# Kernel optimization log

Hardware: AMD Instinct MI355X
Metric: run time of the kernel (lower is better)

Reference implementation:

```python
import jax, jax.numpy as jnp
import numpy as np

B, T, DIM, MDIM, HID = 16, 2048, 1024, 128, 512
WIN = 16
HALF = WIN // 2              # 8 even / 8 odd tokens per window
MAXP = int(0.8 * HALF)       # candidate_ratio * min(nA, nB) = 6 pairs per window
SIM_THRESH = -10.0           # permissive: never masks a cosine similarity
KEEP_RATIO = 0.7
SIM_W, IMP_W, ALPHA_SCALE = 1.0, 0.5, 5.0
LN_EPS = 1e-5


def _ln(x, g, b):
    mu = jnp.mean(x, -1, keepdims=True)
    var = jnp.mean((x - mu) ** 2, -1, keepdims=True)
    return (x - mu) / jnp.sqrt(var + LN_EPS) * g + b


def _greedy(s):
    # s: [HALF, HALF] bipartite sims. Greedy conflict-free matching by descending
    # similarity; since min(nA,nB)=8 >= MAXP=6 it always yields exactly MAXP pairs.
    order = jnp.argsort(-s.reshape(-1))

    def body(k, st):
        usedA, usedB, pa, pb, cnt = st
        idx = order[k]
        iA = (idx // HALF).astype(jnp.int32)
        iB = (idx % HALF).astype(jnp.int32)
        ok = (cnt < MAXP) & (~usedA[iA]) & (~usedB[iB])
        usedA = usedA.at[iA].set(usedA[iA] | ok)
        usedB = usedB.at[iB].set(usedB[iB] | ok)
        w = jnp.where(ok, cnt, MAXP)  # slot MAXP is a scratch slot
        pa = pa.at[w].set(jnp.where(ok, iA, pa[w]))
        pb = pb.at[w].set(jnp.where(ok, iB, pb[w]))
        return (usedA, usedB, pa, pb, cnt + ok.astype(jnp.int32))

    st0 = (jnp.zeros(HALF, bool), jnp.zeros(HALF, bool),
           jnp.zeros(MAXP + 1, jnp.int32), jnp.zeros(MAXP + 1, jnp.int32),
           jnp.int32(0))
    _, _, pa, pb, _ = jax.lax.fori_loop(0, HALF * HALF, body, st0)
    pa, pb = pa[:MAXP], pb[:MAXP]
    return pa, pb, s[pa, pb]


def _forward(x, ln_m_g, ln_m_b, w_match, ln_i_g, ln_i_b, w_imp1, b_imp1, w_imp2, b_imp2):
    Bc, Tc, C = x.shape
    nW = Tc // WIN
    P = nW * MAXP
    K = int((1.0 - KEEP_RATIO) * Tc)  # fixed merge budget (top-K)

    # matching space (L2-normalized) and per-token importance
    m = _ln(x, ln_m_g, ln_m_b) @ w_match                      # [B,T,MDIM]
    m = m / jnp.linalg.norm(m, axis=-1, keepdims=True)
    h = jax.nn.relu(_ln(x, ln_i_g, ln_i_b) @ w_imp1 + b_imp1)
    imp = jax.nn.sigmoid((h @ w_imp2 + b_imp2)[..., 0])       # [B,T]

    # windowed even/odd bipartite similarity
    mw = m.reshape(Bc, nW, WIN, MDIM)
    sim = jnp.einsum('bwad,bwcd->bwac', mw[:, :, 0::2], mw[:, :, 1::2])  # [B,nW,8,8]
    sim = jnp.where(sim < SIM_THRESH, -jnp.inf, sim)

    pa, pb, sv = jax.vmap(jax.vmap(_greedy))(sim)             # [B,nW,MAXP]
    wstart = (jnp.arange(nW, dtype=jnp.int32) * WIN)[None, :, None]
    i_idx = (wstart + 2 * pa).reshape(Bc, P)                  # keep token (even)
    j_idx = (wstart + 2 * pb + 1).reshape(Bc, P)              # drop token (odd)
    sim_c = sv.reshape(Bc, P)
    imp_i = jnp.take_along_axis(imp, i_idx, axis=1)
    imp_j = jnp.take_along_axis(imp, j_idx, axis=1)

    # fixed budget: exactly top-K merges by score (high sim, low importance)
    scores = SIM_W * sim_c - IMP_W * 0.5 * (imp_i + imp_j)
    _, top = jax.lax.top_k(scores, K)
    z = jnp.zeros((Bc, P), x.dtype).at[jnp.arange(Bc)[:, None], top].set(1.0)

    # merge keeps i, drops j; alpha from relative importance
    alpha = jax.nn.sigmoid(ALPHA_SCALE * (imp_i - imp_j))[..., None]
    xi = jnp.take_along_axis(x, i_idx[..., None], axis=1)
    xj = jnp.take_along_axis(x, j_idx[..., None], axis=1)
    merged = alpha * xi + (1.0 - alpha) * xj                  # [B,P,C]

    def pack_one(xb, ib, jb, mb, zb):
        # i indices are globally unique -> scatter merged content where z==1
        x_new = xb.at[ib].add(zb[:, None] * (mb - xb[ib]))
        drop = (jnp.zeros(Tc, xb.dtype).at[jb].add(zb)) > 0.5
        # stable argsort keeps surviving tokens in time order; take first T-K
        order = jnp.argsort(drop.astype(jnp.int32))[:Tc - K]
        return x_new[order]

    return jax.vmap(pack_one)(x, i_idx, j_idx, merged, z)     # [B, T-K, C]


def setup_inputs() -> dict:
    key = jax.random.key(0)
    ks = jax.random.split(key, 4)
    s = 0.02
    return {
        'x': jax.random.normal(ks[0], (B, T, DIM), jnp.float32),
        'ln_m_g': jnp.ones((DIM,), jnp.float32),
        'ln_m_b': jnp.zeros((DIM,), jnp.float32),
        'w_match': jax.random.normal(ks[1], (DIM, MDIM), jnp.float32) * s,
        'ln_i_g': jnp.ones((DIM,), jnp.float32),
        'ln_i_b': jnp.zeros((DIM,), jnp.float32),
        'w_imp1': jax.random.normal(ks[2], (DIM, HID), jnp.float32) * s,
        'b_imp1': jnp.zeros((HID,), jnp.float32),
        'w_imp2': jax.random.normal(ks[3], (HID, 1), jnp.float32) * s,
        'b_imp2': jnp.zeros((1,), jnp.float32),
    }


def reference(x, ln_m_g, ln_m_b, w_match, ln_i_g, ln_i_b, w_imp1, b_imp1, w_imp2, b_imp2):
    return _forward(x, ln_m_g, ln_m_b, w_match, ln_i_g, ln_i_b, w_imp1, b_imp1, w_imp2, b_imp2)
```

## Files before the change

### kernel.cpp

```cpp
#include <hip/hip_runtime.h>
#include <math.h>

#define B_ 16
#define T_ 2048
#define DIM_ 1024
#define MDIM_ 128
#define HID_ 512
#define NCAT 640
#define NW_ 128
#define WINSZ 16
#define MAXP_ 6
#define P_ 768
#define KDROP 614
#define TKEEP 1434
#define NTOK (B_*T_)

typedef unsigned short u16;
typedef __bf16 bf16x8 __attribute__((ext_vector_type(8)));
typedef float f32x4 __attribute__((ext_vector_type(4)));
typedef unsigned short us4 __attribute__((ext_vector_type(4)));

#define OFF_WCAT   0
#define OFF_BIAS   (OFF_WCAT + DIM_*NCAT)
#define OFF_MU     (OFF_BIAS + NCAT)
#define OFF_RS     (OFF_MU + NTOK)
#define OFF_MBUF   (OFF_RS + NTOK)
#define OFF_LOGIT  (OFF_MBUF + NTOK*MDIM_)
#define OFF_IMP    (OFF_LOGIT + NTOK)
#define OFF_IIDX   (OFF_IMP + NTOK)
#define OFF_JIDX   (OFF_IIDX + B_*P_)
#define OFF_SV     (OFF_JIDX + B_*P_)
#define OFF_ALPHA  (OFF_SV + B_*P_)
#define OFF_REP    (OFF_ALPHA + B_*P_)
#define OFF_DROP   (OFF_REP + NTOK)
#define OFF_POS    (OFF_DROP + NTOK)

static constexpr size_t F_AH    = 0;
static constexpr size_t F_AL    = F_AH + (size_t)NTOK*DIM_/2;
static constexpr size_t F_BH    = F_AL + (size_t)NTOK*DIM_/2;
static constexpr size_t F_BL    = F_BH + (size_t)NCAT*DIM_/2;
static constexpr size_t F_BIAS  = F_BL + (size_t)NCAT*DIM_/2;
static constexpr size_t F_MBUF  = F_BIAS + NCAT;
static constexpr size_t F_LOGIT = F_MBUF + (size_t)NTOK*MDIM_;
static constexpr size_t F_IMP   = F_LOGIT + NTOK;
static constexpr size_t F_IIDX  = F_IMP + NTOK;
static constexpr size_t F_JIDX  = F_IIDX + (size_t)B_*P_;
static constexpr size_t F_SV    = F_JIDX + (size_t)B_*P_;
static constexpr size_t F_ALPHA = F_SV + (size_t)B_*P_;
static constexpr size_t F_REP   = F_ALPHA + (size_t)B_*P_;
static constexpr size_t F_DROP  = F_REP + NTOK;
static constexpr size_t F_POS   = F_DROP + NTOK;
static constexpr size_t F_TOTAL = F_POS + NTOK;

__device__ __forceinline__ u16 f2bf(float f) {
  unsigned u = __builtin_bit_cast(unsigned, f);
  unsigned r = u + 0x7FFFu + ((u >> 16) & 1u);
  return (u16)(r >> 16);
}
__device__ __forceinline__ float bf2f(u16 h) {
  unsigned u = ((unsigned)h) << 16;
  return __builtin_bit_cast(float, u);
}
__device__ __forceinline__ void gll16(const void* g, void* l) {
  __builtin_amdgcn_global_load_lds((const __attribute__((address_space(1))) void*)g,
                                   (__attribute__((address_space(3))) void*)l, 16, 0, 0);
}


__global__ __launch_bounds__(256) void prep_a(const float* __restrict__ x,
    u16* __restrict__ Ah, u16* __restrict__ Al) {
  int token = blockIdx.x * 4 + (threadIdx.x >> 6);
  int lane = threadIdx.x & 63;
  const float4* xr = (const float4*)(x + (size_t)token * DIM_);
  float4 v[4];
  float sum = 0.f;
#pragma unroll
  for (int it = 0; it < 4; ++it) {
    v[it] = xr[lane + it * 64];
    sum += v[it].x + v[it].y + v[it].z + v[it].w;
  }
  for (int o = 32; o > 0; o >>= 1) sum += __shfl_xor(sum, o);
  float m = sum * (1.f / 1024.f);
  float ss = 0.f;
#pragma unroll
  for (int it = 0; it < 4; ++it) {
    float a = v[it].x - m, b = v[it].y - m, c = v[it].z - m, d = v[it].w - m;
    ss += a * a + b * b + c * c + d * d;
  }
  for (int o = 32; o > 0; o >>= 1) ss += __shfl_xor(ss, o);
  float rsv = 1.0f / sqrtf(ss * (1.f / 1024.f) + 1e-5f);
#pragma unroll
  for (int it = 0; it < 4; ++it) {
    float e[4] = {(v[it].x - m) * rsv, (v[it].y - m) * rsv,
                  (v[it].z - m) * rsv, (v[it].w - m) * rsv};
    us4 hv, lv;
#pragma unroll
    for (int j = 0; j < 4; ++j) {
      u16 h = f2bf(e[j]);
      hv[j] = h;
      lv[j] = f2bf(e[j] - bf2f(h));
    }
    size_t off = (size_t)token * DIM_ + (size_t)(lane + it * 64) * 4;
    *(us4*)&Ah[off] = hv;
    *(us4*)&Al[off] = lv;
  }
}

__global__ __launch_bounds__(256) void prep_b(const float* __restrict__ wm,
    const float* __restrict__ wi, const float* __restrict__ gm,
    const float* __restrict__ gi, u16* __restrict__ Bh, u16* __restrict__ Bl) {
  int e = blockIdx.x * 256 + threadIdx.x;
  if (e >= NCAT * DIM_) return;
  int n = e >> 10, k = e & 1023;
  float wv = (n < MDIM_) ? gm[k] * wm[k * MDIM_ + n]
                         : gi[k] * wi[k * HID_ + (n - MDIM_)];
  u16 h = f2bf(wv);
  Bh[e] = h;
  Bl[e] = f2bf(wv - bf2f(h));
}

__global__ __launch_bounds__(256, 2) void gemm_mfma(
    const u16* __restrict__ Ah, const u16* __restrict__ Al,
    const u16* __restrict__ Bh, const u16* __restrict__ Bl,
    const float* __restrict__ biascat, const float* __restrict__ w2,
    float* __restrict__ mbuf, float* __restrict__ logit) {
  __shared__ __align__(16) u16 sAH[8 * 512];
  __shared__ __align__(16) u16 sAL[8 * 512];
  __shared__ __align__(16) u16 sBH[8 * 512];
  __shared__ __align__(16) u16 sBL[8 * 512];
  const int tid = threadIdx.x;
  const int w = tid >> 6, lane = tid & 63;
  int bid = blockIdx.x;
  int q = bid / 40, rem = bid % 40;
  int ct = rem >> 3, x8 = rem & 7;
  int stripe = x8 + 8 * q;
  const int row0 = stripe * 128, col0 = ct * 128;
  const int wy = w >> 1, wx = w & 1;
  const int m16 = lane & 15, quad = lane >> 4;

  const u16* gA = (w == 0) ? Ah : (w == 1) ? Al : (w == 2) ? Bh : Bl;
  u16* lds0 = ((w == 0) ? sAH : (w == 1) ? sAL : (w == 2) ? sBH : sBL) + lane * 8;
  const int rbase = (w < 2) ? row0 : col0;
  const u16* gsrc0 = gA + (size_t)(rbase + m16) * DIM_ + quad * 8;

  f32x4 acc[4][4] = {};
  for (int k0 = 0; k0 < DIM_; k0 += 32) {
    __syncthreads();
#pragma unroll
    for (int t = 0; t < 8; ++t)
      gll16(gsrc0 + (size_t)t * 16 * DIM_ + k0, lds0 + t * 512);
    __syncthreads();
    bf16x8 ah[4], al[4], bh[4], bl[4];
#pragma unroll
    for (int i = 0; i < 4; ++i) {
      ah[i] = *(const bf16x8*)&sAH[(wy * 4 + i) * 512 + lane * 8];
      al[i] = *(const bf16x8*)&sAL[(wy * 4 + i) * 512 + lane * 8];
      bh[i] = *(const bf16x8*)&sBH[(wx * 4 + i) * 512 + lane * 8];
      bl[i] = *(const bf16x8*)&sBL[(wx * 4 + i) * 512 + lane * 8];
    }
#pragma unroll
    for (int i = 0; i < 4; ++i)
#pragma unroll
      for (int j = 0; j < 4; ++j) {
        acc[i][j] = __builtin_amdgcn_mfma_f32_16x16x32_bf16(ah[i], bh[j], acc[i][j], 0, 0, 0);
        acc[i][j] = __builtin_amdgcn_mfma_f32_16x16x32_bf16(ah[i], bl[j], acc[i][j], 0, 0, 0);
        acc[i][j] = __builtin_amdgcn_mfma_f32_16x16x32_bf16(al[i], bh[j], acc[i][j], 0, 0, 0);
      }
  }
  if (ct == 0) {
#pragma unroll
    for (int i = 0; i < 4; ++i)
#pragma unroll
      for (int j = 0; j < 4; ++j) {
        int col = wx * 64 + j * 16 + m16;
        float bs = biascat[col];
#pragma unroll
        for (int r = 0; r < 4; ++r) {
          int row = row0 + wy * 64 + i * 16 + quad * 4 + r;
          mbuf[(size_t)row * MDIM_ + col] = acc[i][j][r] + bs;
        }
      }
  } else {
#pragma unroll
    for (int i = 0; i < 4; ++i) {
      float part[4] = {0.f, 0.f, 0.f, 0.f};
#pragma unroll
      for (int j = 0; j < 4; ++j) {
        int col = col0 + wx * 64 + j * 16 + m16;
        float bs = biascat[col];
        float wv = w2[col - MDIM_];
#pragma unroll
        for (int r = 0; r < 4; ++r) {
          float v = acc[i][j][r] + bs;
          v = v > 0.f ? v : 0.f;
          part[r] += v * wv;
        }
      }
#pragma unroll
      for (int r = 0; r < 4; ++r) {
        part[r] += __shfl_xor(part[r], 1);
        part[r] += __shfl_xor(part[r], 2);
        part[r] += __shfl_xor(part[r], 4);
        part[r] += __shfl_xor(part[r], 8);
      }
      if (m16 == 0)
#pragma unroll
        for (int r = 0; r < 4; ++r)
          atomicAdd(&logit[row0 + wy * 64 + i * 16 + quad * 4 + r], part[r]);
    }
  }
}


__global__ __launch_bounds__(256) void build_bias(const float* __restrict__ wm,
    const float* __restrict__ wi, const float* __restrict__ bm,
    const float* __restrict__ bi, const float* __restrict__ b1,
    float* __restrict__ biascat) {
  int c = blockIdx.x;
  float s = 0.f;
  for (int k = threadIdx.x; k < DIM_; k += 256)
    s += (c < MDIM_) ? bm[k] * wm[k * MDIM_ + c]
                     : bi[k] * wi[k * HID_ + (c - MDIM_)];
  __shared__ float red[256];
  red[threadIdx.x] = s; __syncthreads();
  for (int o = 128; o > 0; o >>= 1) {
    if (threadIdx.x < o) red[threadIdx.x] += red[threadIdx.x + o];
    __syncthreads();
  }
  if (threadIdx.x == 0)
    biascat[c] = red[0] + ((c >= MDIM_) ? b1[c - MDIM_] : 0.f);
}

__global__ void zero_logit(float* __restrict__ logit) {
  int i = blockIdx.x * 256 + threadIdx.x;
  if (i < NTOK) logit[i] = 0.f;
}

__global__ __launch_bounds__(256) void norm_m(float* __restrict__ mbuf) {
  int token = blockIdx.x * 4 + (threadIdx.x >> 6);
  int lane = threadIdx.x & 63;
  float2* mr = (float2*)(mbuf + (size_t)token * MDIM_);
  float2 v = mr[lane];
  float ss = v.x * v.x + v.y * v.y;
  for (int o = 32; o > 0; o >>= 1) ss += __shfl_xor(ss, o);
  float inv = 1.0f / sqrtf(ss);
  v.x *= inv; v.y *= inv;
  mr[lane] = v;
}

__global__ void imp_kernel(const float* __restrict__ logit,
    const float* __restrict__ b2, float* __restrict__ imp) {
  int i = blockIdx.x * 256 + threadIdx.x;
  if (i < NTOK) {
    float z = logit[i] + b2[0];
    imp[i] = 1.f / (1.f + expf(-z));
  }
}

__global__ __launch_bounds__(256) void simgreedy(const float* __restrict__ mbuf,
    int* __restrict__ ii, int* __restrict__ jj, float* __restrict__ sv) {
  __shared__ __align__(16) float sm[4][16][132];
  int wv = threadIdx.x >> 6, lane = threadIdx.x & 63;
  int win = blockIdx.x * 4 + wv;
  int b = win >> 7, w = win & 127;
  size_t base = ((size_t)b * T_ + w * WINSZ) * MDIM_;
#pragma unroll
  for (int it = 0; it < 8; ++it) {
    int e4 = it * 64 + lane;
    int row = e4 >> 5, c4 = e4 & 31;
    float4 v = *(const float4*)(mbuf + base + (size_t)row * MDIM_ + c4 * 4);
    *(float4*)&sm[wv][row][c4 * 4] = v;
  }
  __syncthreads();
  int a = lane >> 3, c = lane & 7;
  const float* ev = sm[wv][2 * a];
  const float* od = sm[wv][2 * c + 1];
  float s = 0.f;
#pragma unroll
  for (int k = 0; k < MDIM_; ++k) s += ev[k] * od[k];
  if (s < -10.0f) s = -__builtin_inff();
  float v = s;
  bool alive = true;
  int outb = (b * NW_ + w) * MAXP_;
  for (int p = 0; p < MAXP_; ++p) {
    float bv = alive ? v : -__builtin_inff();
    int bi = lane;
    for (int o = 32; o > 0; o >>= 1) {
      float ov = __shfl_xor(bv, o);
      int oi = __shfl_xor(bi, o);
      if (ov > bv || (ov == bv && oi < bi)) { bv = ov; bi = oi; }
    }
    int wa = bi >> 3, wc = bi & 7;
    if (lane == 0) {
      ii[outb + p] = w * WINSZ + 2 * wa;
      jj[outb + p] = w * WINSZ + 2 * wc + 1;
      sv[outb + p] = bv;
    }
    if (a == wa || c == wc) alive = false;
  }
}

__global__ __launch_bounds__(256) void select_kernel(const float* __restrict__ sv,
    const int* __restrict__ ii, const int* __restrict__ jj,
    const float* __restrict__ imp, float* __restrict__ alpha,
    int* __restrict__ rep, int* __restrict__ drop) {
  int b = blockIdx.x, tid = threadIdx.x;
  __shared__ float sc[P_];
  for (int t = tid; t < T_; t += 256) {
    rep[b * T_ + t] = -1;
    drop[b * T_ + t] = 0;
  }
  for (int p = tid; p < P_; p += 256) {
    int i = ii[b * P_ + p], j = jj[b * P_ + p];
    float fi = imp[b * T_ + i], fj = imp[b * T_ + j];
    sc[p] = sv[b * P_ + p] - 0.25f * (fi + fj);
    alpha[b * P_ + p] = 1.f / (1.f + expf(-5.f * (fi - fj)));
  }
  __syncthreads();
  for (int p = tid; p < P_; p += 256) {
    float s = sc[p];
    int cnt = 0;
    for (int q = 0; q < P_; ++q) {
      float t = sc[q];
      cnt += (t > s) || (t == s && q < p);
    }
    if (cnt < KDROP) {
      rep[b * T_ + ii[b * P_ + p]] = p;
      drop[b * T_ + jj[b * P_ + p]] = 1;
    }
  }
}

__global__ __launch_bounds__(64) void prefix_kernel(const int* __restrict__ drop,
    int* __restrict__ pos) {
  int b = blockIdx.x, lane = threadIdx.x;
  const int* dr = drop + b * T_;
  int t0 = lane * 32;
  int s = 0;
  for (int k = 0; k < 32; ++k) s += (dr[t0 + k] ? 0 : 1);
  int incl = s;
  for (int o = 1; o < 64; o <<= 1) {
    int n = __shfl_up(incl, o);
    if (lane >= o) incl += n;
  }
  int run = incl - s;
  int* ps = pos + b * T_;
  for (int k = 0; k < 32; ++k) {
    ps[t0 + k] = run;
    run += (dr[t0 + k] ? 0 : 1);
  }
}

__global__ __launch_bounds__(256) void pack_kernel(const float* __restrict__ x,
    const int* __restrict__ drop, const int* __restrict__ pos,
    const int* __restrict__ rep, const float* __restrict__ alpha,
    const int* __restrict__ jj, float* __restrict__ out) {
  int t = blockIdx.x, b = blockIdx.y;
  if (drop[b * T_ + t]) return;
  int tid = threadIdx.x;
  const float4* xi = (const float4*)(x + ((size_t)b * T_ + t) * DIM_);
  float4 v = xi[tid];
  int p = rep[b * T_ + t];
  if (p >= 0) {
    float a = alpha[b * P_ + p];
    int j = jj[b * P_ + p];
    const float4* xj = (const float4*)(x + ((size_t)b * T_ + j) * DIM_);
    float4 vj = xj[tid];
    v.x = a * v.x + (1.f - a) * vj.x;
    v.y = a * v.y + (1.f - a) * vj.y;
    v.z = a * v.z + (1.f - a) * vj.z;
    v.w = a * v.w + (1.f - a) * vj.w;
  }
  int np = pos[b * T_ + t];
  ((float4*)(out + ((size_t)b * TKEEP + np) * DIM_))[tid] = v;
}


__global__ __launch_bounds__(256) void build_wcat(const float* __restrict__ wm,
    const float* __restrict__ wi, const float* __restrict__ gm,
    const float* __restrict__ gi, float* __restrict__ Wcat) {
  int e = blockIdx.x * 256 + threadIdx.x;
  if (e >= DIM_ * NCAT) return;
  int k = e / NCAT, c = e - k * NCAT;
  float v = (c < MDIM_) ? gm[k] * wm[k * MDIM_ + c]
                        : gi[k] * wi[k * HID_ + (c - MDIM_)];
  Wcat[e] = v;
}

__global__ __launch_bounds__(256) void ln_stats(const float* __restrict__ x,
    float* __restrict__ mu, float* __restrict__ rs) {
  int token = blockIdx.x * 4 + (threadIdx.x >> 6);
  int lane = threadIdx.x & 63;
  const float4* xr = (const float4*)(x + (size_t)token * DIM_);
  float4 v[4];
  float sum = 0.f;
#pragma unroll
  for (int it = 0; it < 4; ++it) {
    v[it] = xr[lane + it * 64];
    sum += v[it].x + v[it].y + v[it].z + v[it].w;
  }
  for (int o = 32; o > 0; o >>= 1) sum += __shfl_xor(sum, o);
  float m = sum * (1.f / 1024.f);
  float ss = 0.f;
#pragma unroll
  for (int it = 0; it < 4; ++it) {
    float a = v[it].x - m, b = v[it].y - m, c = v[it].z - m, d = v[it].w - m;
    ss += a * a + b * b + c * c + d * d;
  }
  for (int o = 32; o > 0; o >>= 1) ss += __shfl_xor(ss, o);
  if (lane == 0) {
    mu[token] = m;
    rs[token] = 1.0f / sqrtf(ss * (1.f / 1024.f) + 1e-5f);
  }
}

__global__ __launch_bounds__(256) void gemm640(const float* __restrict__ x,
    const float* __restrict__ mu, const float* __restrict__ rs,
    const float* __restrict__ Wcat, const float* __restrict__ biascat,
    const float* __restrict__ w2, float* __restrict__ mbuf,
    float* __restrict__ logit) {
  __shared__ __align__(16) float As[16][68];
  __shared__ __align__(16) float Bs[16][68];
  const int tid = threadIdx.x;
  const int row0 = blockIdx.x * 64, col0 = blockIdx.y * 64;
  const int tx = tid & 15, ty = tid >> 4;
  const int arow = tid >> 2, akk = (tid & 3) << 2;
  const int brow = tid >> 4, bnn = (tid & 15) << 2;
  const int t_g = row0 + arow;
  const float tmu = mu[t_g], trs = rs[t_g];
  const float* xrow = x + (size_t)t_g * DIM_ + akk;
  const float* wptr = Wcat + (size_t)brow * NCAT + col0 + bnn;
  float acc[4][4] = {};
  for (int k0 = 0; k0 < DIM_; k0 += 16) {
    float4 av = *(const float4*)(xrow + k0);
    float4 bv = *(const float4*)(wptr + (size_t)k0 * NCAT);
    As[akk + 0][arow] = (av.x - tmu) * trs;
    As[akk + 1][arow] = (av.y - tmu) * trs;
    As[akk + 2][arow] = (av.z - tmu) * trs;
    As[akk + 3][arow] = (av.w - tmu) * trs;
    *(float4*)&Bs[brow][bnn] = bv;
    __syncthreads();
#pragma unroll
    for (int k = 0; k < 16; ++k) {
      float4 a = *(const float4*)&As[k][ty << 2];
      float4 b = *(const float4*)&Bs[k][tx << 2];
      acc[0][0] += a.x * b.x; acc[0][1] += a.x * b.y; acc[0][2] += a.x * b.z; acc[0][3] += a.x * b.w;
      acc[1][0] += a.y * b.x; acc[1][1] += a.y * b.y; acc[1][2] += a.y * b.z; acc[1][3] += a.y * b.w;
      acc[2][0] += a.z * b.x; acc[2][1] += a.z * b.y; acc[2][2] += a.z * b.z; acc[2][3] += a.z * b.w;
      acc[3][0] += a.w * b.x; acc[3][1] += a.w * b.y; acc[3][2] += a.w * b.z; acc[3][3] += a.w * b.w;
    }
    __syncthreads();
  }
  float bias[4];
#pragma unroll
  for (int j = 0; j < 4; ++j) bias[j] = biascat[col0 + (tx << 2) + j];
  if (col0 < MDIM_) {
#pragma unroll
    for (int i = 0; i < 4; ++i) {
      int t = row0 + (ty << 2) + i;
      float4 o;
      o.x = acc[i][0] + bias[0]; o.y = acc[i][1] + bias[1];
      o.z = acc[i][2] + bias[2]; o.w = acc[i][3] + bias[3];
      *(float4*)(mbuf + (size_t)t * MDIM_ + col0 + (tx << 2)) = o;
    }
  } else {
    float w2v[4];
#pragma unroll
    for (int j = 0; j < 4; ++j) w2v[j] = w2[col0 - MDIM_ + (tx << 2) + j];
#pragma unroll
    for (int i = 0; i < 4; ++i) {
      float p = 0.f;
#pragma unroll
      for (int j = 0; j < 4; ++j) {
        float v = acc[i][j] + bias[j];
        v = v > 0.f ? v : 0.f;
        p += v * w2v[j];
      }
      p += __shfl_xor(p, 1); p += __shfl_xor(p, 2);
      p += __shfl_xor(p, 4); p += __shfl_xor(p, 8);
      if (tx == 0) atomicAdd(&logit[row0 + (ty << 2) + i], p);
    }
  }
}

extern "C" void kernel_launch(void* const* d_in, const int* in_sizes, int n_in,
                              void* d_out, int out_size, void* d_ws, size_t ws_size,
                              hipStream_t stream) {
  const float* x    = (const float*)d_in[0];
  const float* gm   = (const float*)d_in[1];
  const float* bm   = (const float*)d_in[2];
  const float* wm   = (const float*)d_in[3];
  const float* gi   = (const float*)d_in[4];
  const float* bi   = (const float*)d_in[5];
  const float* wi   = (const float*)d_in[6];
  const float* b1   = (const float*)d_in[7];
  const float* w2   = (const float*)d_in[8];
  const float* b2   = (const float*)d_in[9];
  float* ws = (float*)d_ws;
  float* out = (float*)d_out;

  if (ws_size >= F_TOTAL * sizeof(float)) {
    u16* Ah = (u16*)(ws + F_AH);
    u16* Al = (u16*)(ws + F_AL);
    u16* Bh = (u16*)(ws + F_BH);
    u16* Bl = (u16*)(ws + F_BL);
    float* bias  = ws + F_BIAS;
    float* mbuf  = ws + F_MBUF;
    float* logit = ws + F_LOGIT;
    float* imp   = ws + F_IMP;
    int* iidx    = (int*)(ws + F_IIDX);
    int* jidx    = (int*)(ws + F_JIDX);
    float* sv    = ws + F_SV;
    float* alpha = ws + F_ALPHA;
    int* rep     = (int*)(ws + F_REP);
    int* drop    = (int*)(ws + F_DROP);
    int* pos     = (int*)(ws + F_POS);

    prep_b<<<(NCAT * DIM_ + 255) / 256, 256, 0, stream>>>(wm, wi, gm, gi, Bh, Bl);
    build_bias<<<NCAT, 256, 0, stream>>>(wm, wi, bm, bi, b1, bias);
    zero_logit<<<NTOK / 256, 256, 0, stream>>>(logit);
    prep_a<<<NTOK / 4, 256, 0, stream>>>(x, Ah, Al);
    gemm_mfma<<<(NTOK / 128) * (NCAT / 128), 256, 0, stream>>>(Ah, Al, Bh, Bl, bias, w2, mbuf, logit);
    norm_m<<<NTOK / 4, 256, 0, stream>>>(mbuf);
    imp_kernel<<<NTOK / 256, 256, 0, stream>>>(logit, b2, imp);
    simgreedy<<<(B_ * NW_) / 4, 256, 0, stream>>>(mbuf, iidx, jidx, sv);
    select_kernel<<<B_, 256, 0, stream>>>(sv, iidx, jidx, imp, alpha, rep, drop);
    prefix_kernel<<<B_, 64, 0, stream>>>(drop, pos);
    dim3 pgrid(T_, B_);
    pack_kernel<<<pgrid, 256, 0, stream>>>(x, drop, pos, rep, alpha, jidx, out);
  } else {
    float* Wcat = ws + OFF_WCAT;
    float* bias = ws + OFF_BIAS;
    float* mu   = ws + OFF_MU;
    float* rs   = ws + OFF_RS;
    float* mbuf = ws + OFF_MBUF;
    float* logit = ws + OFF_LOGIT;
    float* imp  = ws + OFF_IMP;
    int* iidx   = (int*)(ws + OFF_IIDX);
    int* jidx   = (int*)(ws + OFF_JIDX);
    float* sv   = ws + OFF_SV;
    float* alpha = ws + OFF_ALPHA;
    int* rep    = (int*)(ws + OFF_REP);
    int* drop   = (int*)(ws + OFF_DROP);
    int* pos    = (int*)(ws + OFF_POS);

    build_wcat<<<(DIM_ * NCAT + 255) / 256, 256, 0, stream>>>(wm, wi, gm, gi, Wcat);
    build_bias<<<NCAT, 256, 0, stream>>>(wm, wi, bm, bi, b1, bias);
    zero_logit<<<NTOK / 256, 256, 0, stream>>>(logit);
    ln_stats<<<NTOK / 4, 256, 0, stream>>>(x, mu, rs);
    dim3 ggrid(NTOK / 64, NCAT / 64);
    gemm640<<<ggrid, 256, 0, stream>>>(x, mu, rs, Wcat, bias, w2, mbuf, logit);
    norm_m<<<NTOK / 4, 256, 0, stream>>>(mbuf);
    imp_kernel<<<NTOK / 256, 256, 0, stream>>>(logit, b2, imp);
    simgreedy<<<(B_ * NW_) / 4, 256, 0, stream>>>(mbuf, iidx, jidx, sv);
    select_kernel<<<B_, 256, 0, stream>>>(sv, iidx, jidx, imp, alpha, rep, drop);
    prefix_kernel<<<B_, 64, 0, stream>>>(drop, pos);
    dim3 pgrid(T_, B_);
    pack_kernel<<<pgrid, 256, 0, stream>>>(x, drop, pos, rep, alpha, jidx, out);
  }
}
```

Measured before the change: 573.5 us.

## Double-buffer GEMM LDS tiles and fuse small kernels into neighbors

The MFMA GEMM gets double-buffered LDS tiles, so the global-to-LDS load for the next K slice is issued before the current slice's math and one barrier per iteration goes away. Several small kernels are folded into neighbours: weight prep and bias build share one launch, and L2 normalisation moves into simgreedy's shared-memory stage. The sigmoid importance and the prefix scan move into the selection kernel, and zeroing uses hipMemsetAsync. This cuts launch count and global round-trips, at the cost of doubled LDS per GEMM block, which may lower occupancy.

```diff
diff --git a/kernel.cpp b/kernel.cpp
--- a/kernel.cpp
+++ b/kernel.cpp
@@ -26,8 +26,7 @@
 #define OFF_RS     (OFF_MU + NTOK)
 #define OFF_MBUF   (OFF_RS + NTOK)
 #define OFF_LOGIT  (OFF_MBUF + NTOK*MDIM_)
-#define OFF_IMP    (OFF_LOGIT + NTOK)
-#define OFF_IIDX   (OFF_IMP + NTOK)
+#define OFF_IIDX   (OFF_LOGIT + NTOK)
 #define OFF_JIDX   (OFF_IIDX + B_*P_)
 #define OFF_SV     (OFF_JIDX + B_*P_)
 #define OFF_ALPHA  (OFF_SV + B_*P_)
@@ -42,8 +41,7 @@
 static constexpr size_t F_BIAS  = F_BL + (size_t)NCAT*DIM_/2;
 static constexpr size_t F_MBUF  = F_BIAS + NCAT;
 static constexpr size_t F_LOGIT = F_MBUF + (size_t)NTOK*MDIM_;
-static constexpr size_t F_IMP   = F_LOGIT + NTOK;
-static constexpr size_t F_IIDX  = F_IMP + NTOK;
+static constexpr size_t F_IIDX  = F_LOGIT + NTOK;
 static constexpr size_t F_JIDX  = F_IIDX + (size_t)B_*P_;
 static constexpr size_t F_SV    = F_JIDX + (size_t)B_*P_;
 static constexpr size_t F_ALPHA = F_SV + (size_t)B_*P_;
@@ -106,17 +104,36 @@
   }
 }
 
-__global__ __launch_bounds__(256) void prep_b(const float* __restrict__ wm,
+__global__ __launch_bounds__(256) void prep_w(const float* __restrict__ wm,
     const float* __restrict__ wi, const float* __restrict__ gm,
-    const float* __restrict__ gi, u16* __restrict__ Bh, u16* __restrict__ Bl) {
-  int e = blockIdx.x * 256 + threadIdx.x;
-  if (e >= NCAT * DIM_) return;
-  int n = e >> 10, k = e & 1023;
-  float wv = (n < MDIM_) ? gm[k] * wm[k * MDIM_ + n]
-                         : gi[k] * wi[k * HID_ + (n - MDIM_)];
-  u16 h = f2bf(wv);
-  Bh[e] = h;
-  Bl[e] = f2bf(wv - bf2f(h));
+    const float* __restrict__ gi, const float* __restrict__ bm,
+    const float* __restrict__ bi, const float* __restrict__ b1,
+    u16* __restrict__ Bh, u16* __restrict__ Bl, float* __restrict__ biascat) {
+  int bid = blockIdx.x;
+  const int NBLK_B = (NCAT * DIM_) / 256;
+  if (bid < NBLK_B) {
+    int e = bid * 256 + threadIdx.x;
+    int n = e >> 10, k = e & 1023;
+    float wv = (n < MDIM_) ? gm[k] * wm[k * MDIM_ + n]
+                           : gi[k] * wi[k * HID_ + (n - MDIM_)];
+    u16 h = f2bf(wv);
+    Bh[e] = h;
+    Bl[e] = f2bf(wv - bf2f(h));
+  } else {
+    int c = bid - NBLK_B;
+    float s = 0.f;
+    for (int k = threadIdx.x; k < DIM_; k += 256)
+      s += (c < MDIM_) ? bm[k] * wm[k * MDIM_ + c]
+                       : bi[k] * wi[k * HID_ + (c - MDIM_)];
+    __shared__ float red[256];
+    red[threadIdx.x] = s; __syncthreads();
+    for (int o = 128; o > 0; o >>= 1) {
+      if (threadIdx.x < o) red[threadIdx.x] += red[threadIdx.x + o];
+      __syncthreads();
+    }
+    if (threadIdx.x == 0)
+      biascat[c] = red[0] + ((c >= MDIM_) ? b1[c - MDIM_] : 0.f);
+  }
 }
 
 __global__ __launch_bounds__(256, 2) void gemm_mfma(
@@ -124,10 +141,10 @@
     const u16* __restrict__ Bh, const u16* __restrict__ Bl,
     const float* __restrict__ biascat, const float* __restrict__ w2,
     float* __restrict__ mbuf, float* __restrict__ logit) {
-  __shared__ __align__(16) u16 sAH[8 * 512];
-  __shared__ __align__(16) u16 sAL[8 * 512];
-  __shared__ __align__(16) u16 sBH[8 * 512];
-  __shared__ __align__(16) u16 sBL[8 * 512];
+  __shared__ __align__(16) u16 sAH[2][8 * 512];
+  __shared__ __align__(16) u16 sAL[2][8 * 512];
+  __shared__ __align__(16) u16 sBH[2][8 * 512];
+  __shared__ __align__(16) u16 sBL[2][8 * 512];
   const int tid = threadIdx.x;
   const int w = tid >> 6, lane = tid & 63;
   int bid = blockIdx.x;
@@ -139,24 +156,32 @@
   const int m16 = lane & 15, quad = lane >> 4;
 
   const u16* gA = (w == 0) ? Ah : (w == 1) ? Al : (w == 2) ? Bh : Bl;
-  u16* lds0 = ((w == 0) ? sAH : (w == 1) ? sAL : (w == 2) ? sBH : sBL) + lane * 8;
+  u16* lds0 = ((w == 0) ? sAH[0] : (w == 1) ? sAL[0] : (w == 2) ? sBH[0] : sBL[0]) + lane * 8;
+  u16* lds1 = ((w == 0) ? sAH[1] : (w == 1) ? sAL[1] : (w == 2) ? sBH[1] : sBL[1]) + lane * 8;
   const int rbase = (w < 2) ? row0 : col0;
   const u16* gsrc0 = gA + (size_t)(rbase + m16) * DIM_ + quad * 8;
 
+#pragma unroll
+  for (int t = 0; t < 8; ++t)
+    gll16(gsrc0 + (size_t)t * 16 * DIM_, lds0 + t * 512);
+
   f32x4 acc[4][4] = {};
-  for (int k0 = 0; k0 < DIM_; k0 += 32) {
+  for (int k0 = 0; k0 < 32; ++k0) {
     __syncthreads();
-#pragma unroll
-    for (int t = 0; t < 8; ++t)
-      gll16(gsrc0 + (size_t)t * 16 * DIM_ + k0, lds0 + t * 512);
-    __syncthreads();
+    if (k0 + 1 < 32) {
+      u16* nb = (k0 & 1) ? lds0 : lds1;
+#pragma unroll
+      for (int t = 0; t < 8; ++t)
+        gll16(gsrc0 + (size_t)t * 16 * DIM_ + (k0 + 1) * 32, nb + t * 512);
+    }
+    const int cb = k0 & 1;
     bf16x8 ah[4], al[4], bh[4], bl[4];
 #pragma unroll
     for (int i = 0; i < 4; ++i) {
-      ah[i] = *(const bf16x8*)&sAH[(wy * 4 + i) * 512 + lane * 8];
-      al[i] = *(const bf16x8*)&sAL[(wy * 4 + i) * 512 + lane * 8];
-      bh[i] = *(const bf16x8*)&sBH[(wx * 4 + i) * 512 + lane * 8];
-      bl[i] = *(const bf16x8*)&sBL[(wx * 4 + i) * 512 + lane * 8];
+      ah[i] = *(const bf16x8*)&sAH[cb][(wy * 4 + i) * 512 + lane * 8];
+      al[i] = *(const bf16x8*)&sAL[cb][(wy * 4 + i) * 512 + lane * 8];
+      bh[i] = *(const bf16x8*)&sBH[cb][(wx * 4 + i) * 512 + lane * 8];
+      bl[i] = *(const bf16x8*)&sBL[cb][(wx * 4 + i) * 512 + lane * 8];
     }
 #pragma unroll
     for (int i = 0; i < 4; ++i)
@@ -212,51 +237,6 @@
 }
 
 
-__global__ __launch_bounds__(256) void build_bias(const float* __restrict__ wm,
-    const float* __restrict__ wi, const float* __restrict__ bm,
-    const float* __restrict__ bi, const float* __restrict__ b1,
-    float* __restrict__ biascat) {
-  int c = blockIdx.x;
-  float s = 0.f;
-  for (int k = threadIdx.x; k < DIM_; k += 256)
-    s += (c < MDIM_) ? bm[k] * wm[k * MDIM_ + c]
-                     : bi[k] * wi[k * HID_ + (c - MDIM_)];
-  __shared__ float red[256];
-  red[threadIdx.x] = s; __syncthreads();
-  for (int o = 128; o > 0; o >>= 1) {
-    if (threadIdx.x < o) red[threadIdx.x] += red[threadIdx.x + o];
-    __syncthreads();
-  }
-  if (threadIdx.x == 0)
-    biascat[c] = red[0] + ((c >= MDIM_) ? b1[c - MDIM_] : 0.f);
-}
-
-__global__ void zero_logit(float* __restrict__ logit) {
-  int i = blockIdx.x * 256 + threadIdx.x;
-  if (i < NTOK) logit[i] = 0.f;
-}
-
-__global__ __launch_bounds__(256) void norm_m(float* __restrict__ mbuf) {
-  int token = blockIdx.x * 4 + (threadIdx.x >> 6);
-  int lane = threadIdx.x & 63;
-  float2* mr = (float2*)(mbuf + (size_t)token * MDIM_);
-  float2 v = mr[lane];
-  float ss = v.x * v.x + v.y * v.y;
-  for (int o = 32; o > 0; o >>= 1) ss += __shfl_xor(ss, o);
-  float inv = 1.0f / sqrtf(ss);
-  v.x *= inv; v.y *= inv;
-  mr[lane] = v;
-}
-
-__global__ void imp_kernel(const float* __restrict__ logit,
-    const float* __restrict__ b2, float* __restrict__ imp) {
-  int i = blockIdx.x * 256 + threadIdx.x;
-  if (i < NTOK) {
-    float z = logit[i] + b2[0];
-    imp[i] = 1.f / (1.f + expf(-z));
-  }
-}
-
 __global__ __launch_bounds__(256) void simgreedy(const float* __restrict__ mbuf,
     int* __restrict__ ii, int* __restrict__ jj, float* __restrict__ sv) {
   __shared__ __align__(16) float sm[4][16][132];
@@ -270,6 +250,19 @@
     int row = e4 >> 5, c4 = e4 & 31;
     float4 v = *(const float4*)(mbuf + base + (size_t)row * MDIM_ + c4 * 4);
     *(float4*)&sm[wv][row][c4 * 4] = v;
+  }
+  __syncthreads();
+  {
+    int row = lane >> 2, seg = lane & 3;
+    float* r = sm[wv][row] + seg * 32;
+    float ss = 0.f;
+#pragma unroll
+    for (int k = 0; k < 32; ++k) ss += r[k] * r[k];
+    ss += __shfl_xor(ss, 1);
+    ss += __shfl_xor(ss, 2);
+    float inv = 1.0f / sqrtf(ss);
+#pragma unroll
+    for (int k = 0; k < 32; ++k) r[k] *= inv;
   }
   __syncthreads();
   int a = lane >> 3, c = lane & 7;
@@ -300,19 +293,24 @@
   }
 }
 
-__global__ __launch_bounds__(256) void select_kernel(const float* __restrict__ sv,
+__global__ __launch_bounds__(256) void select_fused(const float* __restrict__ sv,
     const int* __restrict__ ii, const int* __restrict__ jj,
-    const float* __restrict__ imp, float* __restrict__ alpha,
-    int* __restrict__ rep, int* __restrict__ drop) {
+    const float* __restrict__ logit, const float* __restrict__ b2,
+    float* __restrict__ alpha, int* __restrict__ rep,
+    int* __restrict__ drop, int* __restrict__ pos) {
   int b = blockIdx.x, tid = threadIdx.x;
   __shared__ float sc[P_];
+  __shared__ int sdrop[T_];
+  __shared__ int wtot[4];
+  float bb = b2[0];
   for (int t = tid; t < T_; t += 256) {
+    sdrop[t] = 0;
     rep[b * T_ + t] = -1;
-    drop[b * T_ + t] = 0;
   }
   for (int p = tid; p < P_; p += 256) {
     int i = ii[b * P_ + p], j = jj[b * P_ + p];
-    float fi = imp[b * T_ + i], fj = imp[b * T_ + j];
+    float fi = 1.f / (1.f + expf(-(logit[b * T_ + i] + bb)));
+    float fj = 1.f / (1.f + expf(-(logit[b * T_ + j] + bb)));
     sc[p] = sv[b * P_ + p] - 0.25f * (fi + fj);
     alpha[b * P_ + p] = 1.f / (1.f + expf(-5.f * (fi - fj)));
   }
@@ -326,28 +324,31 @@
     }
     if (cnt < KDROP) {
       rep[b * T_ + ii[b * P_ + p]] = p;
-      drop[b * T_ + jj[b * P_ + p]] = 1;
-    }
-  }
-}
-
-__global__ __launch_bounds__(64) void prefix_kernel(const int* __restrict__ drop,
-    int* __restrict__ pos) {
-  int b = blockIdx.x, lane = threadIdx.x;
-  const int* dr = drop + b * T_;
-  int t0 = lane * 32;
+      sdrop[jj[b * P_ + p]] = 1;
+    }
+  }
+  __syncthreads();
+  int base = tid * 8;
+  int loc[8];
   int s = 0;
-  for (int k = 0; k < 32; ++k) s += (dr[t0 + k] ? 0 : 1);
+#pragma unroll
+  for (int k = 0; k < 8; ++k) { loc[k] = s; s += (sdrop[base + k] ? 0 : 1); }
+  int lane = tid & 63, wvi = tid >> 6;
   int incl = s;
   for (int o = 1; o < 64; o <<= 1) {
     int n = __shfl_up(incl, o);
     if (lane >= o) incl += n;
   }
-  int run = incl - s;
-  int* ps = pos + b * T_;
-  for (int k = 0; k < 32; ++k) {
-    ps[t0 + k] = run;
-    run += (dr[t0 + k] ? 0 : 1);
+  if (lane == 63) wtot[wvi] = incl;
+  __syncthreads();
+  int carry = 0;
+  for (int ww = 0; ww < wvi; ++ww) carry += wtot[ww];
+  int excl = carry + incl - s;
+#pragma unroll
+  for (int k = 0; k < 8; ++k) {
+    int t = base + k;
+    drop[b * T_ + t] = sdrop[t];
+    pos[b * T_ + t] = excl + loc[k];
   }
 }
 
@@ -385,6 +386,25 @@
   float v = (c < MDIM_) ? gm[k] * wm[k * MDIM_ + c]
                         : gi[k] * wi[k * HID_ + (c - MDIM_)];
   Wcat[e] = v;
+}
+
+__global__ __launch_bounds__(256) void build_bias(const float* __restrict__ wm,
+    const float* __restrict__ wi, const float* __restrict__ bm,
+    const float* __restrict__ bi, const float* __restrict__ b1,
+    float* __restrict__ biascat) {
+  int c = blockIdx.x;
+  float s = 0.f;
+  for (int k = threadIdx.x; k < DIM_; k += 256)
+    s += (c < MDIM_) ? bm[k] * wm[k * MDIM_ + c]
+                     : bi[k] * wi[k * HID_ + (c - MDIM_)];
+  __shared__ float red[256];
+  red[threadIdx.x] = s; __syncthreads();
+  for (int o = 128; o > 0; o >>= 1) {
+    if (threadIdx.x < o) red[threadIdx.x] += red[threadIdx.x + o];
+    __syncthreads();
+  }
+  if (threadIdx.x == 0)
+    biascat[c] = red[0] + ((c >= MDIM_) ? b1[c - MDIM_] : 0.f);
 }
 
 __global__ __launch_bounds__(256) void ln_stats(const float* __restrict__ x,
@@ -507,7 +527,6 @@
     float* bias  = ws + F_BIAS;
     float* mbuf  = ws + F_MBUF;
     float* logit = ws + F_LOGIT;
-    float* imp   = ws + F_IMP;
     int* iidx    = (int*)(ws + F_IIDX);
     int* jidx    = (int*)(ws + F_JIDX);
     float* sv    = ws + F_SV;
@@ -516,16 +535,12 @@
     int* drop    = (int*)(ws + F_DROP);
     int* pos     = (int*)(ws + F_POS);
 
-    prep_b<<<(NCAT * DIM_ + 255) / 256, 256, 0, stream>>>(wm, wi, gm, gi, Bh, Bl);
-    build_bias<<<NCAT, 256, 0, stream>>>(wm, wi, bm, bi, b1, bias);
-    zero_logit<<<NTOK / 256, 256, 0, stream>>>(logit);
+    hipMemsetAsync(logit, 0, NTOK * sizeof(float), stream);
+    prep_w<<<(NCAT * DIM_) / 256 + NCAT, 256, 0, stream>>>(wm, wi, gm, gi, bm, bi, b1, Bh, Bl, bias);
     prep_a<<<NTOK / 4, 256, 0, stream>>>(x, Ah, Al);
     gemm_mfma<<<(NTOK / 128) * (NCAT / 128), 256, 0, stream>>>(Ah, Al, Bh, Bl, bias, w2, mbuf, logit);
-    norm_m<<<NTOK / 4, 256, 0, stream>>>(mbuf);
-    imp_kernel<<<NTOK / 256, 256, 0, stream>>>(logit, b2, imp);
     simgreedy<<<(B_ * NW_) / 4, 256, 0, stream>>>(mbuf, iidx, jidx, sv);
-    select_kernel<<<B_, 256, 0, stream>>>(sv, iidx, jidx, imp, alpha, rep, drop);
-    prefix_kernel<<<B_, 64, 0, stream>>>(drop, pos);
+    select_fused<<<B_, 256, 0, stream>>>(sv, iidx, jidx, logit, b2, alpha, rep, drop, pos);
     dim3 pgrid(T_, B_);
     pack_kernel<<<pgrid, 256, 0, stream>>>(x, drop, pos, rep, alpha, jidx, out);
   } else {
@@ -535,7 +550,6 @@
     float* rs   = ws + OFF_RS;
     float* mbuf = ws + OFF_MBUF;
     float* logit = ws + OFF_LOGIT;
-    float* imp  = ws + OFF_IMP;
     int* iidx   = (int*)(ws + OFF_IIDX);
     int* jidx   = (int*)(ws + OFF_JIDX);
     float* sv   = ws + OFF_SV;
@@ -544,17 +558,14 @@
     int* drop   = (int*)(ws + OFF_DROP);
     int* pos    = (int*)(ws + OFF_POS);
 
+    hipMemsetAsync(logit, 0, NTOK * sizeof(float), stream);
     build_wcat<<<(DIM_ * NCAT + 255) / 256, 256, 0, stream>>>(wm, wi, gm, gi, Wcat);
     build_bias<<<NCAT, 256, 0, stream>>>(wm, wi, bm, bi, b1, bias);
-    zero_logit<<<NTOK / 256, 256, 0, stream>>>(logit);
     ln_stats<<<NTOK / 4, 256, 0, stream>>>(x, mu, rs);
     dim3 ggrid(NTOK / 64, NCAT / 64);
     gemm640<<<ggrid, 256, 0, stream>>>(x, mu, rs, Wcat, bias, w2, mbuf, logit);
-    norm_m<<<NTOK / 4, 256, 0, stream>>>(mbuf);
-    imp_kernel<<<NTOK / 256, 256, 0, stream>>>(logit, b2, imp);
     simgreedy<<<(B_ * NW_) / 4, 256, 0, stream>>>(mbuf, iidx, jidx, sv);
-    select_kernel<<<B_, 256, 0, stream>>>(sv, iidx, jidx, imp, alpha, rep, drop);
-    prefix_kernel<<<B_, 64, 0, stream>>>(drop, pos);
+    select_fused<<<B_, 256, 0, stream>>>(sv, iidx, jidx, logit, b2, alpha, rep, drop, pos);
     dim3 pgrid(T_, B_);
     pack_kernel<<<pgrid, 256, 0, stream>>>(x, drop, pos, rep, alpha, jidx, out);
   }
```

Result: faster. 531.2 us (-7.4%).
